# Kernel tuning notes

Hardware: AMD Instinct MI355X
Metric: run time of the kernel (lower is better)

## Reference

```python
import jax, jax.numpy as jnp
import numpy as np

NUM_HEADS = 8
EPS = 1e-5


def _dwconv_cpe(x, w, b, H, W):
    # x: [B,N,C]; depthwise 3x3 conv positional encoding with residual
    B, N, C = x.shape
    f = x.transpose(0, 2, 1).reshape(B, C, H, W)
    f = jax.lax.conv_general_dilated(
        f, w, window_strides=(1, 1), padding='SAME',
        feature_group_count=C, dimension_numbers=('NCHW', 'OIHW', 'NCHW'))
    f = f + b[None, :, None, None]
    return x + f.reshape(B, C, N).transpose(0, 2, 1)


def _layernorm(x, g, b):
    mu = jnp.mean(x, axis=-1, keepdims=True)
    var = jnp.mean(jnp.square(x - mu), axis=-1, keepdims=True)
    return (x - mu) * jax.lax.rsqrt(var + EPS) * g + b


def _channel_attn(x, source, q_w, kv_w, proj_w, proj_b):
    B, N, C = x.shape
    h = NUM_HEADS
    d = C // h
    scale = d ** -0.5
    q = (x @ q_w).reshape(B, N, h, d).transpose(0, 2, 1, 3)          # [B,h,N,d]
    kv = (source @ kv_w).reshape(B, N, 2, h, d).transpose(2, 0, 3, 1, 4)
    k = kv[0] * scale                                                # [B,h,N,d]
    v = kv[1]                                                        # [B,h,N,d]
    # channel cross-covariance: [B,h,d,d], softmax over last channel dim
    attn = jax.nn.softmax(jnp.einsum('bhnd,bhne->bhde', k, v), axis=-1)
    out = jnp.einsum('bhde,bhne->bhnd', attn, q)                     # [B,h,N,d]
    out = out.transpose(0, 2, 1, 3).reshape(B, N, C)
    return out @ proj_w + proj_b


def _forward(x, source, H, W, cpe0_w, cpe0_b, cpe1_w, cpe1_b,
             norm1_g, norm1_b, q_w, kv_w, proj_w, proj_b,
             norm2_g, norm2_b, fc1_w, fc1_b, fc2_w, fc2_b):
    x = _dwconv_cpe(x, cpe0_w, cpe0_b, H, W)
    source = _dwconv_cpe(source, cpe0_w, cpe0_b, H, W)  # cpe[0] shared, per source
    x = _layernorm(x, norm1_g, norm1_b)
    source = _layernorm(source, norm1_g, norm1_b)
    cur = _channel_attn(x, source, q_w, kv_w, proj_w, proj_b)
    x = x + cur  # residual on the normalized x (as in the original code)
    x = _dwconv_cpe(x, cpe1_w, cpe1_b, H, W)
    h = _layernorm(x, norm2_g, norm2_b)
    h = jax.nn.gelu(h @ fc1_w + fc1_b, approximate=False) @ fc2_w + fc2_b
    return x + h


def setup_inputs() -> dict:
    key = jax.random.key(0)
    ks = jax.random.split(key, 16)
    B, H, W, C = 8, 64, 64, 384
    N = H * W
    Ch = int(C * 4.0)
    s = 0.02
    return {
        'x': jax.random.normal(ks[0], (B, N, C), jnp.float32),
        'source': jax.random.normal(ks[1], (B, N, C), jnp.float32),
        'H': H, 'W': W,
        'cpe0_w': jax.random.normal(ks[2], (C, 1, 3, 3), jnp.float32) * s,
        'cpe0_b': jnp.zeros((C,), jnp.float32),
        'cpe1_w': jax.random.normal(ks[3], (C, 1, 3, 3), jnp.float32) * s,
        'cpe1_b': jnp.zeros((C,), jnp.float32),
        'norm1_g': jnp.ones((C,), jnp.float32),
        'norm1_b': jnp.zeros((C,), jnp.float32),
        'q_w': jax.random.normal(ks[4], (C, C), jnp.float32) * s,
        'kv_w': jax.random.normal(ks[5], (C, 2 * C), jnp.float32) * s,
        'proj_w': jax.random.normal(ks[6], (C, C), jnp.float32) * s,
        'proj_b': jnp.zeros((C,), jnp.float32),
        'norm2_g': jnp.ones((C,), jnp.float32),
        'norm2_b': jnp.zeros((C,), jnp.float32),
        'fc1_w': jax.random.normal(ks[7], (C, Ch), jnp.float32) * s,
        'fc1_b': jnp.zeros((Ch,), jnp.float32),
        'fc2_w': jax.random.normal(ks[8], (Ch, C), jnp.float32) * s,
        'fc2_b': jnp.zeros((C,), jnp.float32),
    }


def reference(x, source, H, W, cpe0_w, cpe0_b, cpe1_w, cpe1_b,
              norm1_g, norm1_b, q_w, kv_w, proj_w, proj_b,
              norm2_g, norm2_b, fc1_w, fc1_b, fc2_w, fc2_b):
    return _forward(x, source, H, W, cpe0_w, cpe0_b, cpe1_w, cpe1_b,
                    norm1_g, norm1_b, q_w, kv_w, proj_w, proj_b,
                    norm2_g, norm2_b, fc1_w, fc1_b, fc2_w, fc2_b)
```

## Files before the change

### kernel.cpp

```cpp
#include <hip/hip_runtime.h>
#include <hip/hip_bf16.h>
#include <math.h>

typedef __hip_bfloat16 bf16;
typedef unsigned short u16t;
typedef __bf16 bfx8 __attribute__((ext_vector_type(8)));
typedef float fx4 __attribute__((ext_vector_type(4)));
typedef unsigned short usx8 __attribute__((ext_vector_type(8)));

constexpr int Bq = 8, Hh = 64, Ww = 64, Nn = 4096, Cc = 384, NH = 8, CH = 1536;
constexpr int Mrows = Bq * Nn;
constexpr int NS = 4;
constexpr float EPSC = 1e-5f;
constexpr float SCALE = 0.14433756729740643f;

__device__ __forceinline__ float toF(bf16 v) { return __bfloat162float(v); }

__device__ __forceinline__ float ldFlag(const void* p, size_t i, int f) {
    if (f) return __bfloat162float(((const bf16*)p)[i]);
    return ((const float*)p)[i];
}

__device__ __forceinline__ float u2f(u16t u) {
    unsigned int x = ((unsigned int)u) << 16;
    float fv;
    __builtin_memcpy(&fv, &x, 4);
    return fv;
}
__device__ __forceinline__ u16t f2u(float v) {
    bf16 h = __float2bfloat16(v);
    u16t u;
    __builtin_memcpy(&u, &h, 2);
    return u;
}
__device__ __forceinline__ fx4 mfma16(usx8 a, usx8 b, fx4 c) {
    return __builtin_amdgcn_mfma_f32_16x16x32_bf16(
        __builtin_bit_cast(bfx8, a), __builtin_bit_cast(bfx8, b), c, 0, 0, 0);
}

__global__ __launch_bounds__(256) void probe_k(const void* __restrict__ p, int* __restrict__ flag) {
    int t = threadIdx.x;
    int bad = 0;
    for (int i = t; i < 4096; i += 256) {
        unsigned short u = ((const unsigned short*)p)[i];
        unsigned e = (u >> 7) & 0xFF;
        if (e >= 134) bad++;
    }
    __shared__ int sh[256];
    sh[t] = bad;
    __syncthreads();
    for (int s = 128; s > 0; s >>= 1) {
        if (t < s) sh[t] += sh[t + s];
        __syncthreads();
    }
    if (t == 0) flag[0] = (sh[0] < 64) ? 1 : 0;
}

__global__ __launch_bounds__(384) void prep_k(const void* __restrict__ g,
                                              const void* __restrict__ b,
                                              u16t* __restrict__ gB, u16t* __restrict__ bB,
                                              const int* __restrict__ flagp) {
    int f = *flagp;
    int t = threadIdx.x;
    gB[t] = f2u(ldFlag(g, t, f));
    bB[t] = f2u(ldFlag(b, t, f));
}

template <int INM, int MODE>
__global__ __launch_bounds__(384) void dwconv_ln(const void* __restrict__ xin,
                                                 const void* __restrict__ w,
                                                 const void* __restrict__ bias,
                                                 bf16* __restrict__ out,
                                                 const void* __restrict__ g,
                                                 const void* __restrict__ bb,
                                                 float* __restrict__ mu,
                                                 float* __restrict__ rs,
                                                 const int* __restrict__ flagp) {
    int f = *flagp;
    int c = threadIdx.x;
    int w0 = blockIdx.x * 8;
    int hh = blockIdx.y;
    int b = blockIdx.z;
    size_t base = (size_t)b * Nn * Cc;
    float wreg[9];
#pragma unroll
    for (int j = 0; j < 9; j++) wreg[j] = ldFlag(w, c * 9 + j, f);
    float bc = ldFlag(bias, c, f);
    float v[3][10];
#pragma unroll
    for (int ky = 0; ky < 3; ky++) {
        int yy = hh + ky - 1;
        bool rv = (yy >= 0 && yy < Hh);
#pragma unroll
        for (int j = 0; j < 10; j++) {
            int xx = w0 - 1 + j;
            bool cv = (xx >= 0 && xx < Ww);
            float val = 0.f;
            if (rv && cv) {
                size_t idx = base + (size_t)(yy * Ww + xx) * Cc + c;
                val = (INM == 1) ? toF(((const bf16*)xin)[idx]) : ldFlag(xin, idx, f);
            }
            v[ky][j] = val;
        }
    }
    float r[8], s[8], s2[8];
#pragma unroll
    for (int p = 0; p < 8; p++) {
        float a = bc;
#pragma unroll
        for (int ky = 0; ky < 3; ky++)
#pragma unroll
            for (int kx = 0; kx < 3; kx++) a += v[ky][p + kx] * wreg[ky * 3 + kx];
        r[p] = v[1][p + 1] + a;
        s[p] = r[p];
        s2[p] = r[p] * r[p];
    }
#pragma unroll
    for (int off = 32; off > 0; off >>= 1) {
#pragma unroll
        for (int p = 0; p < 8; p++) {
            s[p] += __shfl_down(s[p], off, 64);
            s2[p] += __shfl_down(s2[p], off, 64);
        }
    }
    __shared__ float shS[6][8], shS2[6][8];
    __shared__ float shMu[8], shRs[8];
    int wv = c >> 6, ln = c & 63;
    if (ln == 0) {
#pragma unroll
        for (int p = 0; p < 8; p++) {
            shS[wv][p] = s[p];
            shS2[wv][p] = s2[p];
        }
    }
    __syncthreads();
    if (c < 8) {
        float S = 0, S2 = 0;
#pragma unroll
        for (int q = 0; q < 6; q++) {
            S += shS[q][c];
            S2 += shS2[q][c];
        }
        float m = S * (1.0f / Cc);
        float var = S2 * (1.0f / Cc) - m * m;
        float rr = rsqrtf(var + EPSC);
        if (MODE == 0) {
            shMu[c] = m;
            shRs[c] = rr;
        } else {
            int row = b * Nn + hh * Ww + w0 + c;
            mu[row] = m;
            rs[row] = rr;
        }
    }
    if (MODE == 0) {
        __syncthreads();
        float gc = ldFlag(g, c, f), bbc = ldFlag(bb, c, f);
#pragma unroll
        for (int p = 0; p < 8; p++) {
            size_t oi = base + (size_t)(hh * Ww + w0 + p) * Cc + c;
            out[oi] = __float2bfloat16((r[p] - shMu[p]) * shRs[p] * gc + bbc);
        }
    } else {
#pragma unroll
        for (int p = 0; p < 8; p++) {
            size_t oi = base + (size_t)(hh * Ww + w0 + p) * Cc + c;
            out[oi] = __float2bfloat16(r[p]);
        }
    }
}

template <int AM, int OM, int WM, bool GELU, bool LNA, int RES, int AR>
__global__ __launch_bounds__(256) void gemm_k(const void* __restrict__ A, size_t aBatch,
                                              const void* __restrict__ W, size_t wBatch,
                                              int ldw, int colOff,
                                              const void* __restrict__ bias,
                                              const bf16* __restrict__ resid, size_t rBatch,
                                              const float* __restrict__ mu,
                                              const float* __restrict__ rs, size_t sBatch,
                                              const void* __restrict__ cg,
                                              const void* __restrict__ cb,
                                              void* __restrict__ out, size_t oBatch,
                                              size_t outRow0,
                                              int M, int K, int Nc,
                                              const int* __restrict__ flagp) {
    int f = *flagp;
    int z = blockIdx.z;
    const size_t MK = (size_t)M * K;
    __shared__ float As[16][68];
    __shared__ float Bs[16][68];
    int t = threadIdx.x;
    int tx = t & 15, ty = t >> 4;
    int row0 = blockIdx.x * 64, n0 = blockIdx.y * 64;
    float acc[4][4] = {};
    for (int k0 = 0; k0 < K; k0 += 16) {
#pragma unroll
        for (int i = 0; i < 4; i++) {
            int lin = i * 256 + t;
            int kk = lin & 15, m = lin >> 4;
            size_t ai = (size_t)z * aBatch + (size_t)(row0 + m) * K + k0 + kk;
            float v;
            if (AR > 1) {
                v = 0;
#pragma unroll
                for (int s = 0; s < AR; s++) v += ((const float*)A)[ai + (size_t)s * MK];
            } else {
                v = (AM == 0) ? ((const float*)A)[ai] : toF(((const bf16*)A)[ai]);
            }
            if (LNA) {
                float muv = mu[z * sBatch + row0 + m], rsv = rs[z * sBatch + row0 + m];
                v = (v - muv) * rsv * ldFlag(cg, k0 + kk, f) + ldFlag(cb, k0 + kk, f);
            }
            As[kk][m] = v;
        }
#pragma unroll
        for (int i = 0; i < 4; i++) {
            int lin = i * 256 + t;
            int nn2 = lin & 63, kk = lin >> 6;
            size_t wi = (size_t)z * wBatch + (size_t)(k0 + kk) * ldw + colOff + n0 + nn2;
            Bs[kk][nn2] = (WM == 1) ? toF(((const bf16*)W)[wi]) : ldFlag(W, wi, f);
        }
        __syncthreads();
#pragma unroll
        for (int kk = 0; kk < 16; kk++) {
            float a[4], bv[4];
#pragma unroll
            for (int i = 0; i < 4; i++) a[i] = As[kk][ty * 4 + i];
#pragma unroll
            for (int j = 0; j < 4; j++) bv[j] = Bs[kk][tx * 4 + j];
#pragma unroll
            for (int i = 0; i < 4; i++)
#pragma unroll
                for (int j = 0; j < 4; j++) acc[i][j] += a[i] * bv[j];
        }
        __syncthreads();
    }
#pragma unroll
    for (int i = 0; i < 4; i++) {
        int m = row0 + ty * 4 + i;
#pragma unroll
        for (int j = 0; j < 4; j++) {
            int nn2 = n0 + tx * 4 + j;
            float v = acc[i][j];
            if (bias) v += ldFlag(bias, nn2, f);
            if (GELU) v = 0.5f * v * (1.0f + erff(v * 0.70710678118654752f));
            if (RES == 1) v += toF(resid[(size_t)z * rBatch + (size_t)m * Nc + nn2]);
            size_t oi = (size_t)z * oBatch + (outRow0 + m) * (size_t)Nc + nn2;
            if (OM == 2) ((float*)out)[oi] = v;
            else if (OM == 1) ((bf16*)out)[oi] = __float2bfloat16(v);
            else {
                if (f) ((bf16*)out)[oi] = __float2bfloat16(v);
                else ((float*)out)[oi] = v;
            }
        }
    }
}

__global__ __launch_bounds__(256) void transpose_k(const void* __restrict__ W,
                                                   u16t* __restrict__ WT,
                                                   int K, int N,
                                                   const int* __restrict__ flagp) {
    int f = *flagp;
    __shared__ u16t T[64][72];
    int n0 = blockIdx.x * 64, k0 = blockIdx.y * 64;
    int t = threadIdx.x;
#pragma unroll
    for (int i = 0; i < 16; i++) {
        int lin = i * 256 + t;
        int kk = lin >> 6, nn = lin & 63;
        T[nn][kk] = f2u(ldFlag(W, (size_t)(k0 + kk) * N + n0 + nn, f));
    }
    __syncthreads();
#pragma unroll
    for (int i = 0; i < 16; i++) {
        int lin = i * 256 + t;
        int nn = lin >> 6, kk = lin & 63;
        WT[(size_t)(n0 + nn) * K + k0 + kk] = T[nn][kk];
    }
}

template <int AMODE, int OM, bool GELU, int RES>
__global__ __launch_bounds__(256) void gemm_mfma(
    const u16t* __restrict__ A, size_t aBatch,
    const u16t* __restrict__ BT, size_t btBatch,
    const void* __restrict__ bias,
    const u16t* __restrict__ resid, size_t rBatch,
    const float* __restrict__ mu, const float* __restrict__ rs, size_t sBatch,
    const u16t* __restrict__ gbf, const u16t* __restrict__ bbf,
    void* __restrict__ out, size_t oBatch, size_t outRow0,
    int K, int N, const int* __restrict__ flagp) {
    int f = *flagp;
    int z = blockIdx.z;
    int t = threadIdx.x;
    int row0 = blockIdx.x * 128, n0 = blockIdx.y * 128;
    __shared__ u16t As[128][64];
    __shared__ u16t Bs[128][64];
    const u16t* Ab = A + (size_t)z * aBatch;
    const u16t* Bb = BT + (size_t)z * btBatch;
    const int sm = t >> 3;
    const int sk8 = t & 7;
    float muv[4], rsv[4];
    if (AMODE == 1) {
#pragma unroll
        for (int i = 0; i < 4; i++) {
            int m = row0 + i * 32 + sm;
            muv[i] = mu[(size_t)z * sBatch + m];
            rsv[i] = rs[(size_t)z * sBatch + m];
        }
    }
    usx8 ra[4], rb[4];
    auto ldstep = [&](int k0) {
#pragma unroll
        for (int i = 0; i < 4; i++) {
            ra[i] = *(const usx8*)&Ab[(size_t)(row0 + i * 32 + sm) * K + k0 + sk8 * 8];
            rb[i] = *(const usx8*)&Bb[(size_t)(n0 + i * 32 + sm) * K + k0 + sk8 * 8];
        }
    };
    auto wrstep = [&](int k0) {
        usx8 ga, ba;
        if (AMODE == 1) {
            ga = *(const usx8*)&gbf[k0 + sk8 * 8];
            ba = *(const usx8*)&bbf[k0 + sk8 * 8];
        }
#pragma unroll
        for (int i = 0; i < 4; i++) {
            int row = i * 32 + sm;
            int dst = (sk8 ^ (row & 7)) << 3;
            if (AMODE == 1) {
                usx8 v;
#pragma unroll
                for (int j = 0; j < 8; j++)
                    v[j] = f2u((u2f(ra[i][j]) - muv[i]) * rsv[i] * u2f(ga[j]) + u2f(ba[j]));
                *(usx8*)&As[row][dst] = v;
            } else {
                *(usx8*)&As[row][dst] = ra[i];
            }
            *(usx8*)&Bs[row][dst] = rb[i];
        }
    };
    fx4 acc[4][4];
    fx4 zz = {0.f, 0.f, 0.f, 0.f};
#pragma unroll
    for (int i = 0; i < 4; i++)
#pragma unroll
        for (int j = 0; j < 4; j++) acc[i][j] = zz;
    int lane = t & 63, w = t >> 6;
    int wr = (w >> 1) * 64, wc = (w & 1) * 64;
    int lr = lane & 15, lg = lane >> 4;
    ldstep(0);
    wrstep(0);
    __syncthreads();
    int KT = K / 64;
    for (int kt = 0; kt < KT; kt++) {
        if (kt + 1 < KT) ldstep((kt + 1) * 64);
#pragma unroll
        for (int ks = 0; ks < 2; ks++) {
            usx8 af[4], bfv[4];
#pragma unroll
            for (int r = 0; r < 4; r++) {
                int row = wr + r * 16 + lr;
                af[r] = *(const usx8*)&As[row][((4 * ks + lg) ^ (row & 7)) << 3];
            }
#pragma unroll
            for (int c = 0; c < 4; c++) {
                int row = wc + c * 16 + lr;
                bfv[c] = *(const usx8*)&Bs[row][((4 * ks + lg) ^ (row & 7)) << 3];
            }
#pragma unroll
            for (int r = 0; r < 4; r++)
#pragma unroll
                for (int c = 0; c < 4; c++)
                    acc[r][c] = mfma16(af[r], bfv[c], acc[r][c]);
        }
        __syncthreads();
        if (kt + 1 < KT) {
            wrstep((kt + 1) * 64);
            __syncthreads();
        }
    }
#pragma unroll
    for (int r = 0; r < 4; r++) {
#pragma unroll
        for (int c = 0; c < 4; c++) {
            int gc = n0 + wc + c * 16 + lr;
            float bv = bias ? ldFlag(bias, gc, f) : 0.0f;
#pragma unroll
            for (int q = 0; q < 4; q++) {
                int m = row0 + wr + r * 16 + lg * 4 + q;
                float v = acc[r][c][q] + bv;
                if (GELU) v = 0.5f * v * (1.0f + erff(v * 0.70710678118654752f));
                if (RES == 1) v += u2f(resid[(size_t)z * rBatch + (size_t)m * N + gc]);
                if (RES == 2) v += u2f(Ab[(size_t)m * K + gc]);
                size_t oi = (size_t)z * oBatch + (outRow0 + m) * (size_t)N + gc;
                if (OM == 1) ((u16t*)out)[oi] = f2u(v);
                else {
                    if (f) ((u16t*)out)[oi] = f2u(v);
                    else ((float*)out)[oi] = v;
                }
            }
        }
    }
}

__global__ __launch_bounds__(256) void gram_mfma(const u16t* __restrict__ sc,
                                                 float* __restrict__ Gp) {
    int bx = blockIdx.x, sp = blockIdx.y, b = blockIdx.z;
    int ci0 = (bx / 3) * 128, cj0 = (bx % 3) * 128;
    __shared__ u16t As[128][72];
    __shared__ u16t Bs[128][72];
    int t = threadIdx.x;
    const int scc = (t * 8) & 127;
    const int snn = t >> 4;
    const int RPS = Nn / NS;
    int rowbase = b * Nn + sp * RPS;
    usx8 ra[4], rb[4];
    auto ldstep = [&](int nn0) {
#pragma unroll
        for (int i = 0; i < 4; i++) {
            int r = rowbase + nn0 + i * 16 + snn;
            ra[i] = *(const usx8*)&sc[(size_t)r * Cc + ci0 + scc];
            rb[i] = *(const usx8*)&sc[(size_t)r * Cc + cj0 + scc];
        }
    };
    auto wrstep = [&]() {
#pragma unroll
        for (int i = 0; i < 4; i++) {
            int n = i * 16 + snn;
            int q = n >> 3, nl = n & 7;
#pragma unroll
            for (int j = 0; j < 8; j++) {
                int c = scc + j;
                int swz = ((c >> 3) ^ (c >> 6)) & 7;
                int po = ((q ^ swz) << 3) + nl;
                As[c][po] = ra[i][j];
                Bs[c][po] = rb[i][j];
            }
        }
    };
    fx4 acc[4][4];
    fx4 zz = {0.f, 0.f, 0.f, 0.f};
#pragma unroll
    for (int i = 0; i < 4; i++)
#pragma unroll
        for (int j = 0; j < 4; j++) acc[i][j] = zz;
    int lane = t & 63, w = t >> 6;
    int wr = (w >> 1) * 64, wc = (w & 1) * 64;
    int lr = lane & 15, lg = lane >> 4;
    ldstep(0);
    wrstep();
    __syncthreads();
    const int KT = RPS / 64;
    for (int kt = 0; kt < KT; kt++) {
        if (kt + 1 < KT) ldstep((kt + 1) * 64);
#pragma unroll
        for (int ks = 0; ks < 2; ks++) {
            usx8 af[4], bfv[4];
#pragma unroll
            for (int r = 0; r < 4; r++) {
                int ch = wr + r * 16 + lr;
                int swz = ((ch >> 3) ^ (ch >> 6)) & 7;
                af[r] = *(const usx8*)&As[ch][((ks * 4 + lg) ^ swz) << 3];
            }
#pragma unroll
            for (int c = 0; c < 4; c++) {
                int ch = wc + c * 16 + lr;
                int swz = ((ch >> 3) ^ (ch >> 6)) & 7;
                bfv[c] = *(const usx8*)&Bs[ch][((ks * 4 + lg) ^ swz) << 3];
            }
#pragma unroll
            for (int r = 0; r < 4; r++)
#pragma unroll
                for (int c = 0; c < 4; c++)
                    acc[r][c] = mfma16(af[r], bfv[c], acc[r][c]);
        }
        __syncthreads();
        if (kt + 1 < KT) {
            wrstep();
            __syncthreads();
        }
    }
    float* dst = Gp + ((size_t)b * NS + sp) * (size_t)Cc * Cc;
#pragma unroll
    for (int r = 0; r < 4; r++)
#pragma unroll
        for (int c = 0; c < 4; c++)
#pragma unroll
            for (int q = 0; q < 4; q++)
                dst[(size_t)(ci0 + wr + r * 16 + lg * 4 + q) * Cc + cj0 + wc + c * 16 + lr] =
                    acc[r][c][q];
}

__global__ __launch_bounds__(256) void attn_s_k(const float* __restrict__ P,
                                                const void* __restrict__ kv_w,
                                                float* __restrict__ attn,
                                                const int* __restrict__ flagp) {
    int f = *flagp;
    int hd = blockIdx.x;
    int b = blockIdx.y;
    int t = threadIdx.x;
    const float* Pb = P + (size_t)b * Cc * Cc;
    __shared__ float Pc[32][48];
    __shared__ float Wkc[32][48];
    __shared__ float Ss[48][48];
    int obase = t * 9;
    int dj[9], ej[9];
#pragma unroll
    for (int j = 0; j < 9; j++) {
        dj[j] = (obase + j) / 48;
        ej[j] = (obase + j) % 48;
    }
    float acc[9] = {};
    for (int chunk = 0; chunk < 12; chunk++) {
        for (int idx = t; idx < 1536; idx += 256) {
            int r = idx / 48, e = idx % 48;
            int c = chunk * 32 + r;
            Pc[r][e] = Pb[(size_t)c * Cc + hd * 48 + e];
            Wkc[r][e] = ldFlag(kv_w, (size_t)c * 768 + hd * 48 + e, f);
        }
        __syncthreads();
        for (int r = 0; r < 32; r++) {
#pragma unroll
            for (int j = 0; j < 9; j++) acc[j] += Wkc[r][dj[j]] * Pc[r][ej[j]];
        }
        __syncthreads();
    }
#pragma unroll
    for (int j = 0; j < 9; j++) Ss[dj[j]][ej[j]] = acc[j] * SCALE;
    __syncthreads();
    if (t < 48) {
        float m = -1e30f;
#pragma unroll
        for (int e = 0; e < 48; e++) m = fmaxf(m, Ss[t][e]);
        float ex[48];
        float sum = 0;
#pragma unroll
        for (int e = 0; e < 48; e++) {
            ex[e] = expf(Ss[t][e] - m);
            sum += ex[e];
        }
        float inv = 1.0f / sum;
#pragma unroll
        for (int e = 0; e < 48; e++)
            attn[((size_t)b * NH + hd) * 2304 + t * 48 + e] = ex[e] * inv;
    }
}

__global__ __launch_bounds__(256) void wtilde_k(const void* __restrict__ q_w,
                                                const float* __restrict__ attn,
                                                bf16* __restrict__ Wt_,
                                                const int* __restrict__ flagp) {
    int f = *flagp;
    int c0 = blockIdx.x * 64;
    int hd = blockIdx.y;
    int b = blockIdx.z;
    int t = threadIdx.x;
    __shared__ float at[48][48];
    __shared__ float wq[64][48];
    const float* ab = attn + ((size_t)b * NH + hd) * 2304;
    for (int o = t; o < 2304; o += 256) at[o / 48][o % 48] = ab[o];
    for (int o = t; o < 3072; o += 256) {
        int cc = o / 48, e = o % 48;
        wq[cc][e] = ldFlag(q_w, (size_t)(c0 + cc) * Cc + hd * 48 + e, f);
    }
    __syncthreads();
    bf16* outb = Wt_ + (size_t)b * Cc * Cc;
    for (int o = t; o < 3072; o += 256) {
        int cc = o / 48, d = o % 48;
        float s = 0;
#pragma unroll
        for (int e = 0; e < 48; e++) s += wq[cc][e] * at[d][e];
        outb[(size_t)(c0 + cc) * Cc + hd * 48 + d] = __float2bfloat16(s);
    }
}

extern "C" void kernel_launch(void* const* d_in, const int* in_sizes, int n_in,
                              void* d_out, int out_size, void* d_ws, size_t ws_size,
                              hipStream_t stream) {
    (void)in_sizes; (void)n_in; (void)out_size;
    const void* x = d_in[0];
    const void* srcp = d_in[1];
    const void* cpe0_w = d_in[4];
    const void* cpe0_b = d_in[5];
    const void* cpe1_w = d_in[6];
    const void* cpe1_b = d_in[7];
    const void* n1g = d_in[8];
    const void* n1b = d_in[9];
    const void* q_w = d_in[10];
    const void* kv_w = d_in[11];
    const void* proj_w = d_in[12];
    const void* proj_b = d_in[13];
    const void* n2g = d_in[14];
    const void* n2b = d_in[15];
    const void* fc1_w = d_in[16];
    const void* fc1_b = d_in[17];
    const void* fc2_w = d_in[18];
    const void* fc2_b = d_in[19];
    char* ws = (char*)d_ws;

    const size_t CcCc = (size_t)Cc * Cc;
    const size_t NnCc = (size_t)Nn * Cc;
    const size_t SLOT = (size_t)Mrows * Cc * sizeof(bf16);
    int* flag = (int*)ws;
    bf16* s0 = (bf16*)(ws + 64);
    bf16* s1 = (bf16*)(ws + 64 + SLOT);
    float* Gp = (float*)s1;
    u16t* WeffT = (u16t*)s1;
    bf16* x3 = s1;
    float* P = (float*)(ws + 64 + 2 * SLOT);
    bf16* Wt_ = (bf16*)P;
    u16t* projT = (u16t*)((char*)P + 2359296);
    u16t* fc1T = (u16t*)P;
    u16t* fc2T = (u16t*)((char*)P + 1179648);
    float* attnB = (float*)(ws + 64 + 2 * SLOT + 4718592);
    float* mu2 = (float*)(ws + 64 + 2 * SLOT + 4718592 + 589824);
    float* rs2 = mu2 + Mrows;
    u16t* gB = (u16t*)(rs2 + Mrows);
    u16t* bB = gB + 384;
    bf16* lnS = s0;
    bf16* x2 = s0;
    u16t* h1c = (u16t*)s0;
    const size_t NEED = (size_t)((char*)(bB + 384) - ws);
    if (ws_size < NEED) return;

    bf16* lnX = (bf16*)d_out;

    probe_k<<<1, 256, 0, stream>>>(x, flag);
    prep_k<<<1, 384, 0, stream>>>(n2g, n2b, gB, bB, flag);

    dwconv_ln<2, 0><<<dim3(Ww / 8, Hh, Bq), 384, 0, stream>>>(
        x, cpe0_w, cpe0_b, lnX, n1g, n1b, nullptr, nullptr, flag);

    dwconv_ln<2, 0><<<dim3(Ww / 8, Hh, Bq), 384, 0, stream>>>(
        srcp, cpe0_w, cpe0_b, lnS, n1g, n1b, nullptr, nullptr, flag);
    gram_mfma<<<dim3(9, NS, Bq), 256, 0, stream>>>((const u16t*)lnS, Gp);

    gemm_k<0, 2, 2, false, false, 0, NS><<<dim3(6, 6, Bq), 256, 0, stream>>>(
        Gp, (size_t)NS * CcCc, kv_w, 0, 768, 384, nullptr, nullptr, 0,
        nullptr, nullptr, 0, nullptr, nullptr, P, CcCc, 0, Cc, Cc, Cc, flag);

    attn_s_k<<<dim3(NH, Bq), 256, 0, stream>>>(P, kv_w, attnB, flag);
    wtilde_k<<<dim3(6, NH, Bq), 256, 0, stream>>>(q_w, attnB, Wt_, flag);
    transpose_k<<<dim3(6, 6), 256, 0, stream>>>(proj_w, projT, Cc, Cc, flag);
    gemm_mfma<0, 1, false, 0><<<dim3(3, 3, Bq), 256, 0, stream>>>(
        projT, 0, (const u16t*)Wt_, CcCc, nullptr, nullptr, 0,
        nullptr, nullptr, 0, nullptr, nullptr, WeffT, CcCc, 0, Cc, Cc, flag);

    transpose_k<<<dim3(24, 6), 256, 0, stream>>>(fc1_w, fc1T, Cc, CH, flag);
    transpose_k<<<dim3(6, 24), 256, 0, stream>>>(fc2_w, fc2T, CH, Cc, flag);

    gemm_mfma<0, 1, false, 2><<<dim3(32, 3, Bq), 256, 0, stream>>>(
        (const u16t*)lnX, NnCc, WeffT, CcCc, proj_b, nullptr, 0,
        nullptr, nullptr, 0, nullptr, nullptr, x2, NnCc, 0, Cc, Cc, flag);

    dwconv_ln<1, 1><<<dim3(Ww / 8, Hh, Bq), 384, 0, stream>>>(
        x2, cpe1_w, cpe1_b, x3, nullptr, nullptr, mu2, rs2, flag);

    constexpr int CR = 8192;
    for (int ch = 0; ch < Mrows / CR; ch++) {
        size_t roff = (size_t)ch * CR;
        gemm_mfma<1, 1, true, 0><<<dim3(CR / 128, CH / 128, 1), 256, 0, stream>>>(
            (const u16t*)x3 + roff * Cc, 0, fc1T, 0, fc1_b, nullptr, 0,
            mu2 + roff, rs2 + roff, 0, gB, bB, h1c, 0, 0, Cc, CH, flag);
        gemm_mfma<0, 0, false, 1><<<dim3(CR / 128, Cc / 128, 1), 256, 0, stream>>>(
            h1c, 0, fc2T, 0, fc2_b, (const u16t*)x3 + roff * Cc, 0,
            nullptr, nullptr, 0, nullptr, nullptr, d_out, 0, roff, CH, Cc, flag);
    }
}
```

Measured before the change: 861.4 us.

## Split attention score reduction across blocks and pre-reduce Gram partials

The attention-score kernel previously ran only 64 blocks, each looping over all 384 channels. It now splits that channel reduction into 6 partial blocks per (head, batch) and adds a separate softmax kernel that sums the partials. The Gram split-K partials are also summed once by a new vectorized reduce kernel, so the following GEMM reads one slice instead of accumulating four. This raises parallelism on small stages in exchange for extra launches and extra global traffic for the partial sums.

```diff
diff --git a/kernel.cpp b/kernel.cpp
--- a/kernel.cpp
+++ b/kernel.cpp
@@ -11,6 +11,7 @@
 constexpr int Bq = 8, Hh = 64, Ww = 64, Nn = 4096, Cc = 384, NH = 8, CH = 1536;
 constexpr int Mrows = Bq * Nn;
 constexpr int NS = 4;
+constexpr int NSP = 6;
 constexpr float EPSC = 1e-5f;
 constexpr float SCALE = 0.14433756729740643f;
 
@@ -168,6 +169,19 @@
             out[oi] = __float2bfloat16(r[p]);
         }
     }
+}
+
+__global__ __launch_bounds__(256) void reduceG_k(float* __restrict__ Gp) {
+    const size_t Q = (size_t)Cc * Cc / 4;
+    size_t j = (size_t)blockIdx.x * 256 + threadIdx.x;
+    int b = (int)(j / Q);
+    size_t i4 = j % Q;
+    fx4* G4 = (fx4*)Gp;
+    size_t base = (size_t)b * NS * Q;
+    fx4 a = G4[base + i4];
+#pragma unroll
+    for (int s = 1; s < NS; s++) a += G4[base + (size_t)s * Q + i4];
+    G4[base + i4] = a;
 }
 
 template <int AM, int OM, int WM, bool GELU, bool LNA, int RES, int AR>
@@ -490,42 +504,54 @@
                     acc[r][c][q];
 }
 
-__global__ __launch_bounds__(256) void attn_s_k(const float* __restrict__ P,
-                                                const void* __restrict__ kv_w,
-                                                float* __restrict__ attn,
-                                                const int* __restrict__ flagp) {
+__global__ __launch_bounds__(256) void attn_part_k(const float* __restrict__ P,
+                                                   const void* __restrict__ kv_w,
+                                                   float* __restrict__ Sp,
+                                                   const int* __restrict__ flagp) {
     int f = *flagp;
     int hd = blockIdx.x;
     int b = blockIdx.y;
+    int sp = blockIdx.z;
+    int c0 = sp * 64;
     int t = threadIdx.x;
     const float* Pb = P + (size_t)b * Cc * Cc;
-    __shared__ float Pc[32][48];
-    __shared__ float Wkc[32][48];
-    __shared__ float Ss[48][48];
+    __shared__ float Pc[64][49];
+    __shared__ float Wkc[64][49];
+    for (int idx = t; idx < 3072; idx += 256) {
+        int r = idx / 48, e = idx % 48;
+        int c = c0 + r;
+        Pc[r][e] = Pb[(size_t)c * Cc + hd * 48 + e];
+        Wkc[r][e] = ldFlag(kv_w, (size_t)c * 768 + hd * 48 + e, f);
+    }
+    __syncthreads();
     int obase = t * 9;
-    int dj[9], ej[9];
-#pragma unroll
-    for (int j = 0; j < 9; j++) {
-        dj[j] = (obase + j) / 48;
-        ej[j] = (obase + j) % 48;
-    }
     float acc[9] = {};
-    for (int chunk = 0; chunk < 12; chunk++) {
-        for (int idx = t; idx < 1536; idx += 256) {
-            int r = idx / 48, e = idx % 48;
-            int c = chunk * 32 + r;
-            Pc[r][e] = Pb[(size_t)c * Cc + hd * 48 + e];
-            Wkc[r][e] = ldFlag(kv_w, (size_t)c * 768 + hd * 48 + e, f);
-        }
-        __syncthreads();
-        for (int r = 0; r < 32; r++) {
-#pragma unroll
-            for (int j = 0; j < 9; j++) acc[j] += Wkc[r][dj[j]] * Pc[r][ej[j]];
-        }
-        __syncthreads();
-    }
-#pragma unroll
-    for (int j = 0; j < 9; j++) Ss[dj[j]][ej[j]] = acc[j] * SCALE;
+#pragma unroll
+    for (int r = 0; r < 64; r++) {
+#pragma unroll
+        for (int j = 0; j < 9; j++) {
+            int d = (obase + j) / 48, e = (obase + j) % 48;
+            acc[j] += Wkc[r][d] * Pc[r][e];
+        }
+    }
+    float* dst = Sp + (((size_t)b * NH + hd) * NSP + sp) * 2304;
+#pragma unroll
+    for (int j = 0; j < 9; j++) dst[obase + j] = acc[j];
+}
+
+__global__ __launch_bounds__(256) void attn_soft_k(const float* __restrict__ Sp,
+                                                   float* __restrict__ attn) {
+    int hd = blockIdx.x;
+    int b = blockIdx.y;
+    int t = threadIdx.x;
+    __shared__ float Ss[48][49];
+    const float* src = Sp + (((size_t)b * NH + hd) * NSP) * 2304;
+    for (int idx = t; idx < 2304; idx += 256) {
+        float s = 0;
+#pragma unroll
+        for (int sp = 0; sp < NSP; sp++) s += src[sp * 2304 + idx];
+        Ss[idx / 48][idx % 48] = s * SCALE;
+    }
     __syncthreads();
     if (t < 48) {
         float m = -1e30f;
@@ -617,6 +643,7 @@
     u16t* gB = (u16t*)(rs2 + Mrows);
     u16t* bB = gB + 384;
     bf16* lnS = s0;
+    float* Sp = (float*)s0;
     bf16* x2 = s0;
     u16t* h1c = (u16t*)s0;
     const size_t NEED = (size_t)((char*)(bB + 384) - ws);
@@ -633,12 +660,14 @@
     dwconv_ln<2, 0><<<dim3(Ww / 8, Hh, Bq), 384, 0, stream>>>(
         srcp, cpe0_w, cpe0_b, lnS, n1g, n1b, nullptr, nullptr, flag);
     gram_mfma<<<dim3(9, NS, Bq), 256, 0, stream>>>((const u16t*)lnS, Gp);
-
-    gemm_k<0, 2, 2, false, false, 0, NS><<<dim3(6, 6, Bq), 256, 0, stream>>>(
+    reduceG_k<<<(Bq * CcCc / 4) / 256, 256, 0, stream>>>(Gp);
+
+    gemm_k<0, 2, 2, false, false, 0, 1><<<dim3(6, 6, Bq), 256, 0, stream>>>(
         Gp, (size_t)NS * CcCc, kv_w, 0, 768, 384, nullptr, nullptr, 0,
         nullptr, nullptr, 0, nullptr, nullptr, P, CcCc, 0, Cc, Cc, Cc, flag);
 
-    attn_s_k<<<dim3(NH, Bq), 256, 0, stream>>>(P, kv_w, attnB, flag);
+    attn_part_k<<<dim3(NH, Bq, NSP), 256, 0, stream>>>(P, kv_w, Sp, flag);
+    attn_soft_k<<<dim3(NH, Bq), 256, 0, stream>>>(Sp, attnB);
     wtilde_k<<<dim3(6, NH, Bq), 256, 0, stream>>>(q_w, attnB, Wt_, flag);
     transpose_k<<<dim3(6, 6), 256, 0, stream>>>(proj_w, projT, Cc, Cc, flag);
     gemm_mfma<0, 1, false, 0><<<dim3(3, 3, Bq), 256, 0, stream>>>(
```

New measurement: 886.9 us. +3.0%, slower.
